# Kernel tuning notes

Hardware: AMD Instinct MI355X
Metric: run time of the kernel (lower is better)

## Reference

```python
import jax, jax.numpy as jnp
import numpy as np

OUT_FEATURES = 4096
IN_FEATURES = 4096
NNZ = 838860
N_COLS = 8192


def setup_inputs() -> dict:
    key = jax.random.key(0)
    k_r, k_c, k_v, k_x = jax.random.split(key, 4)
    rows = jax.random.randint(k_r, (NNZ,), 0, OUT_FEATURES, dtype=jnp.int32)
    cols = jax.random.randint(k_c, (NNZ,), 0, IN_FEATURES, dtype=jnp.int32)
    vals = jax.random.normal(k_v, (NNZ,), dtype=jnp.float32)
    x = jax.random.normal(k_x, (IN_FEATURES, N_COLS), dtype=jnp.float32)
    return {"rows": rows, "cols": cols, "vals": vals, "x": x}


def reference(rows, cols, vals, x):
    # Sparse COO weight W[out, in]; duplicate (row, col) entries sum, matching
    # uncoalesced COO semantics of torch.sparse.mm.
    # Dense scatter + GEMM is the clean, efficient jax expression of the same math.
    W = jnp.zeros((OUT_FEATURES, IN_FEATURES), dtype=vals.dtype).at[rows, cols].add(vals)
    return W @ x  # [out_features, N]
```

## Files before the change

kernel.cpp:

```cpp
#include <hip/hip_runtime.h>

#define OUT_F 4096
#define IN_F  4096
#define NCOLS 8192

#define GM OUT_F
#define GK IN_F
#define GN NCOLS

typedef __attribute__((ext_vector_type(8))) short short8;
typedef __attribute__((ext_vector_type(4))) float f32x4;

__device__ inline unsigned short f2bf(float f) {
    union { float f; unsigned u; } c; c.f = f;
    unsigned u = c.u;
    u += 0x7fffu + ((u >> 16) & 1u);
    return (unsigned short)(u >> 16);
}

__device__ inline void gll16(const void* g, void* l) {
    __builtin_amdgcn_global_load_lds(
        (const __attribute__((address_space(1))) unsigned int*)g,
        (__attribute__((address_space(3))) unsigned int*)l, 16, 0, 0);
}

__global__ void scatter_dense(const int* __restrict__ rows, const int* __restrict__ cols,
                              const float* __restrict__ vals, float* __restrict__ W, int nnz) {
    int i = blockIdx.x * blockDim.x + threadIdx.x;
    if (i < nnz) atomicAdd(&W[(size_t)rows[i] * IN_F + cols[i]], vals[i]);
}

__global__ void convert_w(const float* __restrict__ Wf, unsigned short* __restrict__ Wb) {
    int i = blockIdx.x * blockDim.x + threadIdx.x;
    float4 v = ((const float4*)Wf)[i];
    ushort4 o;
    o.x = f2bf(v.x); o.y = f2bf(v.y); o.z = f2bf(v.z); o.w = f2bf(v.w);
    ((ushort4*)Wb)[i] = o;
}

__global__ __launch_bounds__(256) void transpose_x(const float* __restrict__ x,
                                                   unsigned short* __restrict__ xT) {
    __shared__ float tile[64][65];
    const int k0 = blockIdx.x * 64;
    const int n0 = blockIdx.y * 64;
    const int t = threadIdx.x;
    const int c4 = (t & 15) * 4;
    const int r0 = t >> 4;
    for (int p = 0; p < 4; ++p) {
        int r = r0 + p * 16;
        float4 v = *(const float4*)&x[(size_t)(k0 + r) * NCOLS + n0 + c4];
        tile[r][c4 + 0] = v.x; tile[r][c4 + 1] = v.y;
        tile[r][c4 + 2] = v.z; tile[r][c4 + 3] = v.w;
    }
    __syncthreads();
    const int n  = t >> 2;
    const int ks = (t & 3) * 16;
    unsigned w[8];
    for (int m = 0; m < 8; ++m) {
        unsigned short lo = f2bf(tile[ks + 2 * m + 0][n]);
        unsigned short hi = f2bf(tile[ks + 2 * m + 1][n]);
        w[m] = (unsigned)lo | ((unsigned)hi << 16);
    }
    uint4* dst = (uint4*)&xT[(size_t)(n0 + n) * GK + k0 + ks];
    dst[0] = make_uint4(w[0], w[1], w[2], w[3]);
    dst[1] = make_uint4(w[4], w[5], w[6], w[7]);
}

__global__ __launch_bounds__(512, 2) void gemm256(const unsigned short* __restrict__ A,
                                                  const unsigned short* __restrict__ BT,
                                                  float* __restrict__ C) {
    __shared__ unsigned short lds[8 * 8192];

    const int tid  = threadIdx.x;
    const int wave = tid >> 6;
    const int lane = tid & 63;

    const int wg  = blockIdx.y * 32 + blockIdx.x;
    const int swz = (wg & 7) * 64 + (wg >> 3);
    const int m0  = (swz >> 5) * 256;
    const int n0  = (swz & 31) * 256;

    const int wm = wave >> 2;
    const int wn = wave & 3;

    const int r0s  = tid >> 2;
    const int swz0 = ((tid & 3) ^ ((r0s >> 1) & 3)) << 3;
    const unsigned short* pA0 = A  + (size_t)(m0 + r0s) * GK + swz0;
    const unsigned short* pA1 = pA0 + (size_t)128 * GK;
    const unsigned short* pB0 = BT + (size_t)(n0 + r0s) * GK + swz0;
    const unsigned short* pB1 = pB0 + (size_t)128 * GK;

    const int frow  = lane & 15;
    const int ajb   = ((lane >> 4) ^ ((frow >> 1) & 3)) << 3;
    const int abase = ((wm << 7) + frow) * 32 + ajb;
    const int bbase = ((wn << 6) + frow) * 32 + ajb;

    f32x4 acc[8][4] = {};

#define STAGE_A(bufc, khc, kt_) do {                                            \
        const int koA_ = ((((kt_) & 63) << 6) + ((khc) << 5));                  \
        gll16(pA0 + koA_, &lds[(((bufc) << 2) + (khc)) * 8192 + (wave << 9)]);  \
        gll16(pA1 + koA_, &lds[(((bufc) << 2) + (khc)) * 8192 + 4096 + (wave << 9)]); \
    } while (0)

#define STAGE_B(bufc, khc, kt_) do {                                            \
        const int koB_ = ((((kt_) & 63) << 6) + ((khc) << 5));                  \
        gll16(pB0 + koB_, &lds[(((bufc) << 2) + 2 + (khc)) * 8192 + (wave << 9)]); \
        gll16(pB1 + koB_, &lds[(((bufc) << 2) + 2 + (khc)) * 8192 + 4096 + (wave << 9)]); \
    } while (0)

    STAGE_A(0, 0, 0); STAGE_B(0, 0, 0);
    STAGE_A(0, 1, 0); STAGE_B(0, 1, 0);
    STAGE_A(1, 0, 1); STAGE_B(1, 0, 1);
    asm volatile("s_waitcnt vmcnt(8)" ::: "memory");
    __builtin_amdgcn_s_barrier();

#define KHALF_BLOCK(bufc, khc, STAGE1, STAGE2) do {                             \
        const unsigned short* Ar_ = &lds[(((bufc) << 2) + (khc)) * 8192];       \
        const unsigned short* Br_ = &lds[(((bufc) << 2) + 2 + (khc)) * 8192];   \
        short8 af[4], bf[4];                                                    \
        _Pragma("unroll")                                                       \
        for (int nj = 0; nj < 4; ++nj) bf[nj] = *(const short8*)&Br_[bbase + nj * 512]; \
        _Pragma("unroll")                                                       \
        for (int mi = 0; mi < 4; ++mi) af[mi] = *(const short8*)&Ar_[abase + mi * 512]; \
        STAGE1;                                                                 \
        __builtin_amdgcn_s_barrier();                                           \
        __builtin_amdgcn_s_setprio(1);                                          \
        _Pragma("unroll")                                                       \
        for (int mi = 0; mi < 4; ++mi)                                          \
            _Pragma("unroll")                                                   \
            for (int nj = 0; nj < 4; ++nj)                                      \
                acc[mi][nj] = __builtin_amdgcn_mfma_f32_16x16x32_bf16(          \
                    af[mi], bf[nj], acc[mi][nj], 0, 0, 0);                      \
        __builtin_amdgcn_s_setprio(0);                                          \
        __builtin_amdgcn_s_barrier();                                           \
        _Pragma("unroll")                                                       \
        for (int mi = 0; mi < 4; ++mi) af[mi] = *(const short8*)&Ar_[abase + (4 + mi) * 512]; \
        STAGE2;                                                                 \
        __builtin_amdgcn_s_barrier();                                           \
        __builtin_amdgcn_s_setprio(1);                                          \
        _Pragma("unroll")                                                       \
        for (int mi = 0; mi < 4; ++mi)                                          \
            _Pragma("unroll")                                                   \
            for (int nj = 0; nj < 4; ++nj)                                      \
                acc[4 + mi][nj] = __builtin_amdgcn_mfma_f32_16x16x32_bf16(      \
                    af[mi], bf[nj], acc[4 + mi][nj], 0, 0, 0);                  \
        __builtin_amdgcn_s_setprio(0);                                          \
        asm volatile("s_waitcnt vmcnt(8)" ::: "memory");                        \
        __builtin_amdgcn_s_barrier();                                           \
    } while (0)

#pragma unroll 1
    for (int it = 0; it < GK / 128; ++it) {
        const int kt = it * 2;
        KHALF_BLOCK(0, 0, STAGE_A(1, 1, kt + 1), STAGE_B(1, 1, kt + 1));
        KHALF_BLOCK(0, 1, STAGE_A(0, 0, kt + 2), STAGE_B(0, 0, kt + 2));
        KHALF_BLOCK(1, 0, STAGE_A(0, 1, kt + 2), STAGE_B(0, 1, kt + 2));
        KHALF_BLOCK(1, 1, STAGE_A(1, 0, kt + 3), STAGE_B(1, 0, kt + 3));
    }
#undef KHALF_BLOCK
#undef STAGE_A
#undef STAGE_B

    for (int mi = 0; mi < 8; ++mi) {
        const int r0w = m0 + wm * 128 + mi * 16 + (lane >> 4) * 4;
        for (int nj = 0; nj < 4; ++nj) {
            const int cc = n0 + wn * 64 + nj * 16 + frow;
            for (int r = 0; r < 4; ++r)
                C[(size_t)(r0w + r) * GN + cc] = acc[mi][nj][r];
        }
    }
}

#define WS_COUNTS  0
#define WS_OFFSETS 4097
#define WS_CURSOR  8194
#define WS_HEADER  12290

__global__ void hist_kernel(const int* __restrict__ rows, int* __restrict__ counts, int nnz) {
    int i = blockIdx.x * blockDim.x + threadIdx.x;
    if (i < nnz) atomicAdd(&counts[rows[i]], 1);
}

__global__ void scan_kernel(const int* __restrict__ counts, int* __restrict__ offsets) {
    __shared__ int lsum[256];
    int t = threadIdx.x;
    int base = t * 16;
    int local[16];
    int s = 0;
    for (int i = 0; i < 16; ++i) { local[i] = counts[base + i]; s += local[i]; }
    lsum[t] = s;
    __syncthreads();
    if (t == 0) {
        int acc = 0;
        for (int i = 0; i < 256; ++i) { int v = lsum[i]; lsum[i] = acc; acc += v; }
        offsets[OUT_F] = acc;
    }
    __syncthreads();
    int acc = lsum[t];
    for (int i = 0; i < 16; ++i) { offsets[base + i] = acc; acc += local[i]; }
}

__global__ void scatter_kernel(const int* __restrict__ rows, const int* __restrict__ cols,
                               const float* __restrict__ vals,
                               const int* __restrict__ offsets, int* __restrict__ cursor,
                               int* __restrict__ cols_s, float* __restrict__ vals_s, int nnz) {
    int i = blockIdx.x * blockDim.x + threadIdx.x;
    if (i < nnz) {
        int r = rows[i];
        int pos = offsets[r] + atomicAdd(&cursor[r], 1);
        cols_s[pos] = cols[i];
        vals_s[pos] = vals[i];
    }
}

__global__ __launch_bounds__(256) void spmm_kernel(const int* __restrict__ offsets,
                                                   const int* __restrict__ cols_s,
                                                   const float* __restrict__ vals_s,
                                                   const float* __restrict__ x,
                                                   float* __restrict__ out) {
    const int row  = blockIdx.x;
    const int col0 = blockIdx.y * 1024 + threadIdx.x * 4;
    const int k0 = offsets[row];
    const int k1 = offsets[row + 1];
    float4 acc = make_float4(0.f, 0.f, 0.f, 0.f);
    for (int k = k0; k < k1; ++k) {
        const int   c = cols_s[k];
        const float v = vals_s[k];
        const float4 xv = *reinterpret_cast<const float4*>(x + (size_t)c * NCOLS + col0);
        acc.x += v * xv.x;
        acc.y += v * xv.y;
        acc.z += v * xv.z;
        acc.w += v * xv.w;
    }
    *reinterpret_cast<float4*>(out + (size_t)row * NCOLS + col0) = acc;
}

extern "C" void kernel_launch(void* const* d_in, const int* in_sizes, int n_in,
                              void* d_out, int out_size, void* d_ws, size_t ws_size,
                              hipStream_t stream) {
    const int*   rows = (const int*)d_in[0];
    const int*   cols = (const int*)d_in[1];
    const float* vals = (const float*)d_in[2];
    const float* x    = (const float*)d_in[3];
    float*       out  = (float*)d_out;
    const int nnz = in_sizes[0];

    const size_t WF_BYTES = (size_t)GM * GK * 4;
    const size_t WB_BYTES = (size_t)GM * GK * 2;
    const size_t NEED = WF_BYTES + WB_BYTES;

    if (ws_size >= NEED) {
        float*          Wf = (float*)d_ws;
        unsigned short* Wb = (unsigned short*)((char*)d_ws + WF_BYTES);
        unsigned short* xT = (unsigned short*)d_ws;

        hipMemsetAsync(Wf, 0, WF_BYTES, stream);
        scatter_dense<<<(nnz + 255) / 256, 256, 0, stream>>>(rows, cols, vals, Wf, nnz);
        convert_w<<<(GM * GK / 4) / 256, 256, 0, stream>>>(Wf, Wb);
        dim3 tg(GK / 64, GN / 64);
        transpose_x<<<tg, 256, 0, stream>>>(x, xT);
        dim3 gg(GN / 256, GM / 256);
        gemm256<<<gg, 512, 0, stream>>>(Wb, xT, out);
    } else {
        int*   ws_i    = (int*)d_ws;
        int*   counts  = ws_i + WS_COUNTS;
        int*   offsets = ws_i + WS_OFFSETS;
        int*   cursor  = ws_i + WS_CURSOR;
        int*   cols_s  = ws_i + WS_HEADER;
        float* vals_s  = (float*)(ws_i + WS_HEADER + nnz);

        hipMemsetAsync(d_ws, 0, (size_t)WS_HEADER * sizeof(int), stream);
        const int nblk = (nnz + 255) / 256;
        hist_kernel<<<nblk, 256, 0, stream>>>(rows, counts, nnz);
        scan_kernel<<<1, 256, 0, stream>>>(counts, offsets);
        scatter_kernel<<<nblk, 256, 0, stream>>>(rows, cols, vals, offsets, cursor,
                                                 cols_s, vals_s, nnz);
        dim3 grid(OUT_F, NCOLS / 1024);
        spmm_kernel<<<grid, 256, 0, stream>>>(offsets, cols_s, vals_s, x, out);
    }
}
```

Measured before the change: 541.0 us.

## Restructure GEMM main loop into 4-stage ring with register double-buffered fragments

Replaces the two-buffer, two-khalf scheme with a 4-slot LDS ring where each phase issues one prefetch of A and B for a stage three steps ahead. Fragments for the next stage are loaded into alternate register sets while the current MFMAs run, which cuts barriers from three per k-half to one. The aim is to reduce barrier stalls and hide LDS read latency behind MFMA work. The cost is higher register pressure, and correctness now depends on the vmcnt(4) and ring-reuse timing, including prefetches that wrap past the end of K.

```diff
diff --git a/kernel.cpp b/kernel.cpp
--- a/kernel.cpp
+++ b/kernel.cpp
@@ -69,7 +69,7 @@
 __global__ __launch_bounds__(512, 2) void gemm256(const unsigned short* __restrict__ A,
                                                   const unsigned short* __restrict__ BT,
                                                   float* __restrict__ C) {
-    __shared__ unsigned short lds[8 * 8192];
+    __shared__ unsigned short lds[65536];
 
     const int tid  = threadIdx.x;
     const int wave = tid >> 6;
@@ -97,70 +97,70 @@
 
     f32x4 acc[8][4] = {};
 
-#define STAGE_A(bufc, khc, kt_) do {                                            \
-        const int koA_ = ((((kt_) & 63) << 6) + ((khc) << 5));                  \
-        gll16(pA0 + koA_, &lds[(((bufc) << 2) + (khc)) * 8192 + (wave << 9)]);  \
-        gll16(pA1 + koA_, &lds[(((bufc) << 2) + (khc)) * 8192 + 4096 + (wave << 9)]); \
+#define STAGE(q_, s_) do {                                              \
+        const int ko_ = (((q_) & 127) << 5);                            \
+        gll16(pA0 + ko_, &lds[(s_) * 8192 + (wave << 9)]);              \
+        gll16(pA1 + ko_, &lds[(s_) * 8192 + 4096 + (wave << 9)]);       \
+        gll16(pB0 + ko_, &lds[32768 + (s_) * 8192 + (wave << 9)]);      \
+        gll16(pB1 + ko_, &lds[32768 + (s_) * 8192 + 4096 + (wave << 9)]); \
     } while (0)
 
-#define STAGE_B(bufc, khc, kt_) do {                                            \
-        const int koB_ = ((((kt_) & 63) << 6) + ((khc) << 5));                  \
-        gll16(pB0 + koB_, &lds[(((bufc) << 2) + 2 + (khc)) * 8192 + (wave << 9)]); \
-        gll16(pB1 + koB_, &lds[(((bufc) << 2) + 2 + (khc)) * 8192 + 4096 + (wave << 9)]); \
-    } while (0)
-
-    STAGE_A(0, 0, 0); STAGE_B(0, 0, 0);
-    STAGE_A(0, 1, 0); STAGE_B(0, 1, 0);
-    STAGE_A(1, 0, 1); STAGE_B(1, 0, 1);
+    STAGE(0, 0); STAGE(1, 1); STAGE(2, 2);
     asm volatile("s_waitcnt vmcnt(8)" ::: "memory");
-    __builtin_amdgcn_s_barrier();
-
-#define KHALF_BLOCK(bufc, khc, STAGE1, STAGE2) do {                             \
-        const unsigned short* Ar_ = &lds[(((bufc) << 2) + (khc)) * 8192];       \
-        const unsigned short* Br_ = &lds[(((bufc) << 2) + 2 + (khc)) * 8192];   \
-        short8 af[4], bf[4];                                                    \
-        _Pragma("unroll")                                                       \
-        for (int nj = 0; nj < 4; ++nj) bf[nj] = *(const short8*)&Br_[bbase + nj * 512]; \
-        _Pragma("unroll")                                                       \
-        for (int mi = 0; mi < 4; ++mi) af[mi] = *(const short8*)&Ar_[abase + mi * 512]; \
-        STAGE1;                                                                 \
-        __builtin_amdgcn_s_barrier();                                           \
+    asm volatile("s_barrier" ::: "memory");
+
+    short8 bfX[4], afX[4], bfY[4], afY[4];
+    {
+        const unsigned short* Ar0 = &lds[0];
+        const unsigned short* Br0 = &lds[32768];
+#pragma unroll
+        for (int nj = 0; nj < 4; ++nj) bfX[nj] = *(const short8*)&Br0[bbase + nj * 512];
+#pragma unroll
+        for (int mi = 0; mi < 4; ++mi) afX[mi] = *(const short8*)&Ar0[abase + mi * 512];
+    }
+
+#define PHASE(e_, bfC, afC, bfN, afN, jj) do {                                  \
+        asm volatile("s_waitcnt vmcnt(4)" ::: "memory");                        \
+        asm volatile("s_barrier" ::: "memory");                                 \
+        const unsigned short* ArC = &lds[(e_) * 8192];                          \
+        const unsigned short* ArN = &lds[(((e_) + 1) & 3) * 8192];              \
+        const unsigned short* BrN = &lds[32768 + (((e_) + 1) & 3) * 8192];      \
+        short8 af2[4];                                                          \
+        _Pragma("unroll")                                                       \
+        for (int mi = 0; mi < 4; ++mi)                                          \
+            af2[mi] = *(const short8*)&ArC[abase + (4 + mi) * 512];             \
+        _Pragma("unroll")                                                       \
+        for (int nj = 0; nj < 4; ++nj)                                          \
+            bfN[nj] = *(const short8*)&BrN[bbase + nj * 512];                   \
+        _Pragma("unroll")                                                       \
+        for (int mi = 0; mi < 4; ++mi)                                          \
+            afN[mi] = *(const short8*)&ArN[abase + mi * 512];                   \
+        STAGE(4 * (jj) + (e_) + 3, ((e_) + 3) & 3);                             \
         __builtin_amdgcn_s_setprio(1);                                          \
         _Pragma("unroll")                                                       \
         for (int mi = 0; mi < 4; ++mi)                                          \
             _Pragma("unroll")                                                   \
             for (int nj = 0; nj < 4; ++nj)                                      \
                 acc[mi][nj] = __builtin_amdgcn_mfma_f32_16x16x32_bf16(          \
-                    af[mi], bf[nj], acc[mi][nj], 0, 0, 0);                      \
-        __builtin_amdgcn_s_setprio(0);                                          \
-        __builtin_amdgcn_s_barrier();                                           \
-        _Pragma("unroll")                                                       \
-        for (int mi = 0; mi < 4; ++mi) af[mi] = *(const short8*)&Ar_[abase + (4 + mi) * 512]; \
-        STAGE2;                                                                 \
-        __builtin_amdgcn_s_barrier();                                           \
-        __builtin_amdgcn_s_setprio(1);                                          \
+                    afC[mi], bfC[nj], acc[mi][nj], 0, 0, 0);                    \
         _Pragma("unroll")                                                       \
         for (int mi = 0; mi < 4; ++mi)                                          \
             _Pragma("unroll")                                                   \
             for (int nj = 0; nj < 4; ++nj)                                      \
                 acc[4 + mi][nj] = __builtin_amdgcn_mfma_f32_16x16x32_bf16(      \
-                    af[mi], bf[nj], acc[4 + mi][nj], 0, 0, 0);                  \
+                    af2[mi], bfC[nj], acc[4 + mi][nj], 0, 0, 0);                \
         __builtin_amdgcn_s_setprio(0);                                          \
-        asm volatile("s_waitcnt vmcnt(8)" ::: "memory");                        \
-        __builtin_amdgcn_s_barrier();                                           \
     } while (0)
 
 #pragma unroll 1
-    for (int it = 0; it < GK / 128; ++it) {
-        const int kt = it * 2;
-        KHALF_BLOCK(0, 0, STAGE_A(1, 1, kt + 1), STAGE_B(1, 1, kt + 1));
-        KHALF_BLOCK(0, 1, STAGE_A(0, 0, kt + 2), STAGE_B(0, 0, kt + 2));
-        KHALF_BLOCK(1, 0, STAGE_A(0, 1, kt + 2), STAGE_B(0, 1, kt + 2));
-        KHALF_BLOCK(1, 1, STAGE_A(1, 0, kt + 3), STAGE_B(1, 0, kt + 3));
-    }
-#undef KHALF_BLOCK
-#undef STAGE_A
-#undef STAGE_B
+    for (int j = 0; j < GK / 128; ++j) {
+        PHASE(0, bfX, afX, bfY, afY, j);
+        PHASE(1, bfY, afY, bfX, afX, j);
+        PHASE(2, bfX, afX, bfY, afY, j);
+        PHASE(3, bfY, afY, bfX, afX, j);
+    }
+#undef PHASE
+#undef STAGE
 
     for (int mi = 0; mi < 8; ++mi) {
         const int r0w = m0 + wm * 128 + mi * 16 + (lane >> 4) * 4;
```

Result: faster. 527.3 us (-2.5%).
